# Kernel optimization log

Measured on AMD Instinct MI355X. Metric: run time of the kernel, lower is better.

The kernel has to match this reference:

```python
import jax, jax.numpy as jnp
import numpy as np

B, CIN, MID, OUT = 4096, 64, 256, 256
K = CIN * 25  # flattened 5x5 patch per channel
EPS = 1e-5


def _masks():
    # [3, 25] binary masks over the 5x5 kernel for the 3 branch families
    circle = np.zeros((5, 5), np.float32); circle[1:4, 1:4] = 1.0
    corner = np.zeros((5, 5), np.float32)
    for (i, j) in [(0, 0), (0, 4), (4, 0), (4, 4), (2, 2)]:
        corner[i, j] = 1.0
    horse = np.zeros((5, 5), np.float32)
    for (i, j) in [(0, 1), (0, 3), (1, 0), (1, 4), (3, 0), (3, 4), (4, 1), (4, 3), (2, 2)]:
        horse[i, j] = 1.0
    return jnp.asarray(np.stack([circle, corner, horse]).reshape(3, 25))


def mish(x):
    return x * jnp.tanh(jax.nn.softplus(x))


def setup_inputs() -> dict:
    key = jax.random.key(0)
    ks = jax.random.split(key, 12)
    x = jax.random.normal(ks[0], (B, CIN, 7, 7), jnp.float32)
    W5 = jax.random.normal(ks[1], (27, MID, K), jnp.float32) * 0.05
    b5 = jax.random.normal(ks[2], (27, MID), jnp.float32) * 0.05
    gamma = jnp.ones((27, MID), jnp.float32)
    beta = jnp.zeros((27, MID), jnp.float32)
    run_mean = jax.random.normal(ks[3], (27, MID), jnp.float32) * 0.05
    run_var = jax.random.uniform(ks[4], (27, MID), jnp.float32, 0.5, 1.5)
    W1 = jax.random.normal(ks[5], (27, MID, MID), jnp.float32) * 0.05
    b1 = jax.random.normal(ks[6], (27, MID), jnp.float32) * 0.05
    W2 = jax.random.normal(ks[7], (27, OUT, MID), jnp.float32) * 0.05
    b2 = jax.random.normal(ks[8], (27, OUT), jnp.float32) * 0.05
    return {"x": x, "W5": W5, "b5": b5, "gamma": gamma, "beta": beta,
            "run_mean": run_mean, "run_var": run_var,
            "W1": W1, "b1": b1, "W2": W2, "b2": b2}


def reference(x, W5, b5, gamma, beta, run_mean, run_var, W1, b1, W2, b2):
    masks = _masks()  # [3,25]
    # 9 patches of 5x5: [9, B, CIN*25]
    patches = jnp.stack([x[:, :, k:k + 5, v:v + 5]
                         for k in range(3) for v in range(3)])
    patches = patches.reshape(9, B, K)
    # mask kernels per branch family and group weights as [3,9,MID,K]
    mask_k = jnp.repeat(masks, 9, axis=0)          # [27,25]
    mask_k = jnp.tile(mask_k, (1, CIN))[:, None, :]  # [27,1,CIN*25]
    W5m = (W5 * mask_k).reshape(3, 9, MID, K)
    # masked 5x5 conv on 5x5 patch -> 1x1 == dot product: [3,9,B,MID]
    z = jnp.einsum('pbk,gpmk->gpbm', patches, W5m) + b5.reshape(3, 9, 1, MID)
    # BatchNorm (inference, running stats) + Mish
    inv = jax.lax.rsqrt(run_var.reshape(3, 9, 1, MID) + EPS)
    h = mish((z - run_mean.reshape(3, 9, 1, MID)) * inv
             * gamma.reshape(3, 9, 1, MID) + beta.reshape(3, 9, 1, MID))
    # 1x1 conv + Mish, then final 1x1 conv
    h = mish(jnp.einsum('gpbm,gpnm->gpbn', h, W1.reshape(3, 9, MID, MID))
             + b1.reshape(3, 9, 1, MID))
    o = jnp.einsum('gpbm,gpom->gpbo', h, W2.reshape(3, 9, OUT, MID)) \
        + b2.reshape(3, 9, 1, OUT)                 # [3,9,B,OUT]
    copy_features = o[0].sum(0)                    # sum of 9 circle branches
    jump_features = o[1].sum(0) + o[2].sum(0)      # sum of 18 corner+horse
    # output is 1x1 spatially, so flatten(2).sum(2) is identity on [B,OUT]
    return copy_features * jump_features
```

## Files before the change

kernel.cpp:

```cpp
#include <hip/hip_runtime.h>

typedef __bf16 bf16x8 __attribute__((ext_vector_type(8)));
typedef float f32x4 __attribute__((ext_vector_type(4)));

__constant__ int SL_I[3][9] = {{1,1,1,2,2,2,3,3,3},{0,0,2,4,4,0,0,0,0},{0,0,1,1,2,3,3,4,4}};
__constant__ int SL_J[3][9] = {{1,2,3,1,2,3,1,2,3},{0,4,2,0,4,0,0,0,0},{1,3,0,4,2,0,4,1,3}};
__constant__ int SL_S[3][9] = {{6,7,8,11,12,13,16,17,18},{0,4,12,20,24,0,0,0,0},{1,3,5,9,12,15,19,21,23}};

#define GLDS16(gsrc, ldst)                                                        \
  __builtin_amdgcn_global_load_lds(                                               \
      (const __attribute__((address_space(1))) unsigned int*)(gsrc),              \
      (__attribute__((address_space(3))) unsigned int*)(ldst), 16, 0, 0)

#define SBAR()  asm volatile("s_barrier" ::: "memory")
#define VMW(n)  asm volatile("s_waitcnt vmcnt(" #n ")" ::: "memory")
#define SCB()   __builtin_amdgcn_sched_barrier(0)

static __device__ __forceinline__ unsigned short f2b(float f) {
  return __builtin_bit_cast(unsigned short, (__bf16)f);
}
static __device__ __forceinline__ float b2f(unsigned short u) {
  unsigned int b = ((unsigned int)u) << 16;
  return __builtin_bit_cast(float, b);
}
static __device__ __forceinline__ float mish_f(float x) {
  float u = __expf(x);
  float w = u * (u + 2.0f);
  float r = x * w * __builtin_amdgcn_rcpf(w + 2.0f);
  return (x > 20.0f) ? x : r;
}
static __device__ __forceinline__ int swz8(int c, int r) {
  return ((((c >> 3) ^ (r & 7)) << 3) | (c & 7));
}
static __device__ __forceinline__ int swoff(int c, int r) {
  return (c & ~63) | ((c & 63) ^ ((r & 7) << 3));
}

__global__ __launch_bounds__(256) void prep_x_k(const float* __restrict__ X,
                                                unsigned short* __restrict__ Xb) {
  __shared__ float tile[3136];
  const int b = blockIdx.x;
  const float* xp = X + (size_t)b * 3136;
  for (int i = threadIdx.x; i < 3136; i += 256) tile[i] = xp[i];
  __syncthreads();
  for (int i = threadIdx.x; i < 3136; i += 256) {
    int s = i >> 6, c = i & 63;
    Xb[(size_t)s * 262144 + (size_t)b * 64 + swz8(c, b)] = f2b(tile[c * 49 + s]);
  }
}

__global__ __launch_bounds__(256) void prep_w5_k(const float* __restrict__ W5,
                                                 unsigned short* __restrict__ W5c) {
  int tid = blockIdx.x * 256 + threadIdx.x;
  if (tid >= 497664) return;
  int n  = tid & 127;
  int r1 = tid >> 7;
  int q  = r1 & 7;
  int r2 = r1 >> 3;
  int nt = r2 & 1;
  int r3 = r2 >> 1;
  int u  = r3 % 9;
  int gp = r3 / 9;
  int g = gp / 9;
  int nm = (g == 1) ? 5 : 9;
  if (u >= nm) return;
  int s = SL_S[g][u];
  const float* src = W5 + (size_t)(gp * 256 + nt * 128 + n) * 1600 + s;
  unsigned short* dst = W5c + (size_t)tid * 8;
  float a0 = src[(q * 8 + 0) * 25], a1 = src[(q * 8 + 1) * 25];
  float a2 = src[(q * 8 + 2) * 25], a3 = src[(q * 8 + 3) * 25];
  float a4 = src[(q * 8 + 4) * 25], a5 = src[(q * 8 + 5) * 25];
  float a6 = src[(q * 8 + 6) * 25], a7 = src[(q * 8 + 7) * 25];
  ushort4 v0 = {f2b(a0), f2b(a1), f2b(a2), f2b(a3)};
  ushort4 v1 = {f2b(a4), f2b(a5), f2b(a6), f2b(a7)};
  *(ushort4*)(dst) = v0;
  *(ushort4*)(dst + 4) = v1;
}

__global__ __launch_bounds__(256) void prep_w12_k(const float* __restrict__ W1, const float* __restrict__ W2,
                                                  unsigned short* __restrict__ W1c, unsigned short* __restrict__ W2c) {
  int tid = blockIdx.x * 256 + threadIdx.x;
  if (tid >= 221184) return;
  int n  = tid & 255;
  int q  = (tid >> 8) & 3;
  int kt = (tid >> 10) & 7;
  int gp = tid >> 13;
  size_t src = (size_t)(gp * 256 + n) * 256 + kt * 32 + q * 8;
  float4 a0 = *(const float4*)(W1 + src);
  float4 a1 = *(const float4*)(W1 + src + 4);
  float4 b0 = *(const float4*)(W2 + src);
  float4 b1 = *(const float4*)(W2 + src + 4);
  ushort4 ua0 = {f2b(a0.x), f2b(a0.y), f2b(a0.z), f2b(a0.w)};
  ushort4 ua1 = {f2b(a1.x), f2b(a1.y), f2b(a1.z), f2b(a1.w)};
  ushort4 ub0 = {f2b(b0.x), f2b(b0.y), f2b(b0.z), f2b(b0.w)};
  ushort4 ub1 = {f2b(b1.x), f2b(b1.y), f2b(b1.z), f2b(b1.w)};
  *(ushort4*)(W1c + (size_t)tid * 8) = ua0;
  *(ushort4*)(W1c + (size_t)tid * 8 + 4) = ua1;
  *(ushort4*)(W2c + (size_t)tid * 8) = ub0;
  *(ushort4*)(W2c + (size_t)tid * 8 + 4) = ub1;
}

__global__ __launch_bounds__(256) void prep_bn_k(const float* __restrict__ b5, const float* __restrict__ gamma,
                                                 const float* __restrict__ beta, const float* __restrict__ rmean,
                                                 const float* __restrict__ rvar,
                                                 float* __restrict__ bn_a, float* __restrict__ bn_c) {
  int i = blockIdx.x * 256 + threadIdx.x;
  if (i < 27 * 256) {
    float a = gamma[i] * rsqrtf(rvar[i] + 1e-5f);
    bn_a[i] = a;
    bn_c[i] = (b5[i] - rmean[i]) * a + beta[i];
  }
}

__global__ __launch_bounds__(512) void gemm1_k(const unsigned short* __restrict__ Xb,
                                               const unsigned short* __restrict__ W5c,
                                               const float* __restrict__ bn_a, const float* __restrict__ bn_c,
                                               unsigned short* __restrict__ H) {
  __shared__ unsigned short smem[32768];
  const int t = threadIdx.x;
  const int lane = t & 63;
  const int w = t >> 6;
  const int wm = w >> 2, wn = w & 3;
  const int l15 = lane & 15, l4 = lane >> 4;
  const int sw = l15 & 7;
  const int m0 = blockIdx.x * 128, n0 = blockIdx.y * 128;
  const int nt = blockIdx.y;
  const int gp = blockIdx.z;
  const int g = gp / 9, p = gp - g * 9;
  const int pk = p / 3, pv = p - pk * 3;
  const int nm = (g == 1) ? 5 : 9;

  const f32x4 zero = {0.f, 0.f, 0.f, 0.f};
  f32x4 acc[4][2];
#pragma unroll
  for (int i = 0; i < 4; ++i)
#pragma unroll
    for (int j = 0; j < 2; ++j) acc[i][j] = zero;

  auto STAGE = [&](int pbuf, int u) {
    const int s = (pk + SL_I[g][u]) * 7 + (pv + SL_J[g][u]);
    const unsigned short* srcA = Xb + (size_t)s * 262144 + (size_t)m0 * 64;
    const unsigned short* srcB = W5c + ((size_t)((gp * 9 + u) * 2 + nt)) * 8192;
    unsigned short* dA = smem + pbuf * 16384;
    unsigned short* dB = dA + 8192;
#pragma unroll
    for (int it = 0; it < 2; ++it) {
      int idx = it * 512 + t;
      GLDS16(srcA + idx * 8, dA + idx * 8);
    }
#pragma unroll
    for (int it = 0; it < 2; ++it) {
      int idx = it * 512 + t;
      GLDS16(srcB + idx * 8, dB + idx * 8);
    }
  };

  STAGE(0, 0);
  __syncthreads();
  int cur = 0;
  for (int u = 0; u < nm; ++u) {
    if (u + 1 < nm) STAGE(cur ^ 1, u + 1);
    const unsigned short* lA = smem + cur * 16384;
    const unsigned short* lB = lA + 8192;
#pragma unroll
    for (int kk = 0; kk < 2; ++kk) {
      bf16x8 af[4], bfr[2];
#pragma unroll
      for (int f4 = 0; f4 < 4; ++f4)
        af[f4] = *reinterpret_cast<const bf16x8*>(lA + (wm * 64 + f4 * 16 + l15) * 64 + (((kk * 4 + l4) ^ sw) << 3));
#pragma unroll
      for (int f2 = 0; f2 < 2; ++f2)
        bfr[f2] = *reinterpret_cast<const bf16x8*>(lB + (kk * 4 + l4) * 1024 + (wn * 32 + f2 * 16 + l15) * 8);
#pragma unroll
      for (int i = 0; i < 4; ++i)
#pragma unroll
        for (int j = 0; j < 2; ++j)
          acc[i][j] = __builtin_amdgcn_mfma_f32_16x16x32_bf16(af[i], bfr[j], acc[i][j], 0, 0, 0);
    }
    __syncthreads();
    cur ^= 1;
  }
#pragma unroll
  for (int j = 0; j < 2; ++j) {
    const int col = wn * 32 + j * 16 + l15;
    const float a  = bn_a[gp * 256 + n0 + col];
    const float cc = bn_c[gp * 256 + n0 + col];
#pragma unroll
    for (int i = 0; i < 4; ++i) {
      const int r0 = wm * 64 + i * 16 + l4 * 4;
#pragma unroll
      for (int e = 0; e < 4; ++e) {
        const int r = r0 + e;
        float z = acc[i][j][e] * a + cc;
        smem[r * 128 + (col ^ ((r & 7) << 3))] = f2b(mish_f(z));
      }
    }
  }
  __syncthreads();
  {
    unsigned short* Hg = H + (size_t)gp * 1048576;
#pragma unroll
    for (int it = 0; it < 4; ++it) {
      int idx = it * 512 + t;
      int row = idx >> 4, seg = idx & 15;
      int c8 = (seg * 8) ^ ((row & 7) << 3);
      uint4 v = *(const uint4*)(smem + row * 128 + c8);
      int colout = n0 + (seg >> 3) * 64 + (((seg & 7) ^ (row & 7)) << 3);
      *(uint4*)(Hg + (size_t)(m0 + row) * 256 + colout) = v;
    }
  }
}

__global__ __launch_bounds__(512) void gemm23f_k(const unsigned short* __restrict__ Hb,
                                                 const unsigned short* __restrict__ W1c,
                                                 const unsigned short* __restrict__ W2c,
                                                 const float* __restrict__ b1, const float* __restrict__ b2,
                                                 unsigned short* __restrict__ Obuf) {
  extern __shared__ unsigned short smem[];
  unsigned short* stB = smem;
  unsigned short* stA = smem + 24576;
  unsigned short* h1  = smem + 24576;
  const int t = threadIdx.x;
  const int lane = t & 63;
  const int w = t >> 6;
  const int wm = w >> 2, wn = w & 3;
  const int l15 = lane & 15, l4 = lane >> 4;
  const int sw = l15 & 7;
  const int m0 = blockIdx.x * 64;
  const int gp = blockIdx.y;

  const f32x4 zero = {0.f, 0.f, 0.f, 0.f};
  f32x4 acc[2][4];
#pragma unroll
  for (int i = 0; i < 2; ++i)
#pragma unroll
    for (int j = 0; j < 4; ++j) acc[i][j] = zero;

  auto STAGE_A = [&](int pbuf, int kt64) {
    unsigned short* dA = stA + pbuf * 4096;
    GLDS16(Hb + (size_t)(gp * 4096 + m0 + (t >> 3)) * 256 + kt64 * 64 + (t & 7) * 8, dA + t * 8);
  };
  auto STAGE_B = [&](const unsigned short* Wc, int kt32, int pbuf) {
    unsigned short* dB = stB + pbuf * 8192;
    const unsigned short* src = Wc + ((size_t)(gp * 8 + kt32)) * 8192;
#pragma unroll
    for (int it = 0; it < 2; ++it) {
      int idx = it * 512 + t;
      GLDS16(src + idx * 8, dB + idx * 8);
    }
  };

  STAGE_A(0, 0);
  STAGE_B(W1c, 0, 0);
#pragma unroll
  for (int kt = 0; kt < 8; ++kt) {
    if (kt < 7) STAGE_B(W1c, kt + 1, (kt + 1) % 3);
    if ((kt & 1) == 0 && kt < 6) STAGE_A((kt / 2 + 1) % 3, kt / 2 + 1);
    if (kt < 6) { VMW(3); } else if (kt == 6) { VMW(2); } else { VMW(0); }
    SBAR(); SCB();
    const unsigned short* lA = stA + ((kt >> 1) % 3) * 4096;
    const unsigned short* lB = stB + (kt % 3) * 8192;
    bf16x8 af[2], bfr[4];
#pragma unroll
    for (int f2 = 0; f2 < 2; ++f2)
      af[f2] = *reinterpret_cast<const bf16x8*>(lA + (wm * 32 + f2 * 16 + l15) * 64 + ((((kt & 1) * 4 + l4) ^ sw) << 3));
#pragma unroll
    for (int f4 = 0; f4 < 4; ++f4)
      bfr[f4] = *reinterpret_cast<const bf16x8*>(lB + l4 * 2048 + (wn * 64 + f4 * 16 + l15) * 8);
#pragma unroll
    for (int i = 0; i < 2; ++i)
#pragma unroll
      for (int j = 0; j < 4; ++j)
        acc[i][j] = __builtin_amdgcn_mfma_f32_16x16x32_bf16(af[i], bfr[j], acc[i][j], 0, 0, 0);
  }
  __syncthreads();
  STAGE_B(W2c, 0, 0);
#pragma unroll
  for (int j = 0; j < 4; ++j) {
    const int c = wn * 64 + j * 16 + l15;
    const float bi = b1[gp * 256 + c];
#pragma unroll
    for (int i = 0; i < 2; ++i) {
      const int r0 = wm * 32 + i * 16 + l4 * 4;
#pragma unroll
      for (int e = 0; e < 4; ++e) {
        const int r = r0 + e;
        h1[r * 256 + swoff(c, r)] = f2b(mish_f(acc[i][j][e] + bi));
      }
    }
  }
  __syncthreads();

#pragma unroll
  for (int i = 0; i < 2; ++i)
#pragma unroll
    for (int j = 0; j < 4; ++j) acc[i][j] = zero;
#pragma unroll
  for (int kt = 0; kt < 8; ++kt) {
    if (kt < 7) STAGE_B(W2c, kt + 1, (kt + 1) % 3);
    if (kt < 7) { VMW(2); } else { VMW(0); }
    SBAR(); SCB();
    const unsigned short* lB = stB + (kt % 3) * 8192;
    bf16x8 af[2], bfr[4];
#pragma unroll
    for (int f2 = 0; f2 < 2; ++f2) {
      const int row = wm * 32 + f2 * 16 + l15;
      af[f2] = *reinterpret_cast<const bf16x8*>(
          h1 + row * 256 + (kt >> 1) * 64 + ((((kt & 1) * 4 + l4) ^ sw) << 3));
    }
#pragma unroll
    for (int f4 = 0; f4 < 4; ++f4)
      bfr[f4] = *reinterpret_cast<const bf16x8*>(lB + l4 * 2048 + (wn * 64 + f4 * 16 + l15) * 8);
#pragma unroll
    for (int i = 0; i < 2; ++i)
#pragma unroll
      for (int j = 0; j < 4; ++j)
        acc[i][j] = __builtin_amdgcn_mfma_f32_16x16x32_bf16(af[i], bfr[j], acc[i][j], 0, 0, 0);
  }
  __syncthreads();
  unsigned short* tr = stB;
#pragma unroll
  for (int j = 0; j < 4; ++j) {
    const int c = wn * 64 + j * 16 + l15;
    const float bi = b2[gp * 256 + c];
#pragma unroll
    for (int i = 0; i < 2; ++i) {
      const int r0 = wm * 32 + i * 16 + l4 * 4;
#pragma unroll
      for (int e = 0; e < 4; ++e) {
        const int r = r0 + e;
        tr[r * 256 + swoff(c, r)] = f2b(acc[i][j][e] + bi);
      }
    }
  }
  __syncthreads();
  {
    unsigned short* Og = Obuf + (size_t)gp * 1048576;
#pragma unroll
    for (int it = 0; it < 4; ++it) {
      int idx = it * 512 + t;
      int row = idx >> 5, seg = idx & 31;
      int c8 = swoff(seg * 8, row);
      uint4 v = *(const uint4*)(tr + row * 256 + c8);
      *(uint4*)(Og + (size_t)(m0 + row) * 256 + seg * 8) = v;
    }
  }
}

__global__ __launch_bounds__(256) void final_k(const unsigned short* __restrict__ O, float* __restrict__ out) {
  const size_t base = ((size_t)blockIdx.x * 256 + threadIdx.x) * 8;
  float cs[8], js[8];
#pragma unroll
  for (int e = 0; e < 8; ++e) { cs[e] = 0.f; js[e] = 0.f; }
#pragma unroll
  for (int gp = 0; gp < 27; ++gp) {
    uint4 v = *(const uint4*)(O + (size_t)gp * 1048576 + base);
    const unsigned short* pv = (const unsigned short*)&v;
    if (gp < 9) {
#pragma unroll
      for (int e = 0; e < 8; ++e) cs[e] += b2f(pv[e]);
    } else {
#pragma unroll
      for (int e = 0; e < 8; ++e) js[e] += b2f(pv[e]);
    }
  }
  float4 o0 = {cs[0] * js[0], cs[1] * js[1], cs[2] * js[2], cs[3] * js[3]};
  float4 o1 = {cs[4] * js[4], cs[5] * js[5], cs[6] * js[6], cs[7] * js[7]};
  *(float4*)(out + base) = o0;
  *(float4*)(out + base + 4) = o1;
}

extern "C" void kernel_launch(void* const* d_in, const int* in_sizes, int n_in,
                              void* d_out, int out_size, void* d_ws, size_t ws_size,
                              hipStream_t stream) {
  const float* X     = (const float*)d_in[0];
  const float* W5    = (const float*)d_in[1];
  const float* b5    = (const float*)d_in[2];
  const float* gamma = (const float*)d_in[3];
  const float* beta  = (const float*)d_in[4];
  const float* rmean = (const float*)d_in[5];
  const float* rvar  = (const float*)d_in[6];
  const float* W1    = (const float*)d_in[7];
  const float* b1    = (const float*)d_in[8];
  const float* W2    = (const float*)d_in[9];
  const float* b2    = (const float*)d_in[10];
  float* out = (float*)d_out;
  char* ws = (char*)d_ws;

  unsigned short* W5c  = (unsigned short*)(ws);
  unsigned short* W1c  = (unsigned short*)(ws + 7962624);
  unsigned short* W2c  = (unsigned short*)(ws + 11501568);
  float*          bn_a = (float*)(ws + 15040512);
  float*          bn_c = (float*)(ws + 15068160);
  unsigned short* Xb   = (unsigned short*)(ws + 15095808);
  unsigned short* Hbuf = (unsigned short*)(ws + 40785920);
  unsigned short* Obuf = (unsigned short*)(ws + 97409024);

  (void)hipFuncSetAttribute(reinterpret_cast<const void*>(gemm23f_k),
                            hipFuncAttributeMaxDynamicSharedMemorySize, 81920);

  prep_x_k<<<4096, 256, 0, stream>>>(X, Xb);
  prep_w5_k<<<1944, 256, 0, stream>>>(W5, W5c);
  prep_w12_k<<<864, 256, 0, stream>>>(W1, W2, W1c, W2c);
  prep_bn_k<<<27, 256, 0, stream>>>(b5, gamma, beta, rmean, rvar, bn_a, bn_c);

  gemm1_k<<<dim3(32, 2, 27), 512, 0, stream>>>(Xb, W5c, bn_a, bn_c, Hbuf);
  gemm23f_k<<<dim3(64, 27), 512, 81920, stream>>>(Hbuf, W1c, W2c, b1, b2, Obuf);
  final_k<<<512, 256, 0, stream>>>(Obuf, out);
}
```

Baseline: 159.4 us.

## Split gemm1 K-steps into half-tiles with triple-buffered LDS and vmcnt waits

The prep kernel now writes X in a k-major blocked layout (8-element k-chunks by row) instead of a swizzled row-major layout, so each half-K slice of an A tile is contiguous. In gemm1 each 64-wide K step is split into two 32-wide stages, each loaded with a single global_load_lds per thread into a three-slot LDS ring. It waits on vmcnt with one s_barrier per stage instead of two __syncthreads per double-buffered step. This aims to overlap loads with MFMAs more finely and cut LDS use. It adds more barriers per unit of work and drops the XOR swizzle on A reads, which may bring back bank conflicts.

```diff
diff --git a/kernel.cpp b/kernel.cpp
--- a/kernel.cpp
+++ b/kernel.cpp
@@ -28,9 +28,6 @@
   float w = u * (u + 2.0f);
   float r = x * w * __builtin_amdgcn_rcpf(w + 2.0f);
   return (x > 20.0f) ? x : r;
-}
-static __device__ __forceinline__ int swz8(int c, int r) {
-  return ((((c >> 3) ^ (r & 7)) << 3) | (c & 7));
 }
 static __device__ __forceinline__ int swoff(int c, int r) {
   return (c & ~63) | ((c & 63) ^ ((r & 7) << 3));
@@ -43,9 +40,18 @@
   const float* xp = X + (size_t)b * 3136;
   for (int i = threadIdx.x; i < 3136; i += 256) tile[i] = xp[i];
   __syncthreads();
-  for (int i = threadIdx.x; i < 3136; i += 256) {
-    int s = i >> 6, c = i & 63;
-    Xb[(size_t)s * 262144 + (size_t)b * 64 + swz8(c, b)] = f2b(tile[c * 49 + s]);
+  const int mt = b >> 7, mr = b & 127;
+  for (int i = threadIdx.x; i < 392; i += 256) {
+    int s = i >> 3, oc = i & 7;
+    unsigned short* dst = Xb + ((size_t)((s * 32 + mt) * 8 + oc)) * 1024 + mr * 8;
+    ushort4 v0, v1;
+    int c = oc * 8;
+    v0 = {f2b(tile[(c + 0) * 49 + s]), f2b(tile[(c + 1) * 49 + s]),
+          f2b(tile[(c + 2) * 49 + s]), f2b(tile[(c + 3) * 49 + s])};
+    v1 = {f2b(tile[(c + 4) * 49 + s]), f2b(tile[(c + 5) * 49 + s]),
+          f2b(tile[(c + 6) * 49 + s]), f2b(tile[(c + 7) * 49 + s])};
+    *(ushort4*)(dst) = v0;
+    *(ushort4*)(dst + 4) = v1;
   }
 }
 
@@ -116,19 +122,21 @@
                                                const unsigned short* __restrict__ W5c,
                                                const float* __restrict__ bn_a, const float* __restrict__ bn_c,
                                                unsigned short* __restrict__ H) {
-  __shared__ unsigned short smem[32768];
+  __shared__ unsigned short smem[24576];
   const int t = threadIdx.x;
   const int lane = t & 63;
   const int w = t >> 6;
   const int wm = w >> 2, wn = w & 3;
   const int l15 = lane & 15, l4 = lane >> 4;
-  const int sw = l15 & 7;
-  const int m0 = blockIdx.x * 128, n0 = blockIdx.y * 128;
+  const int mt = blockIdx.x;
+  const int m0 = mt * 128;
   const int nt = blockIdx.y;
+  const int n0 = nt * 128;
   const int gp = blockIdx.z;
   const int g = gp / 9, p = gp - g * 9;
   const int pk = p / 3, pv = p - pk * 3;
   const int nm = (g == 1) ? 5 : 9;
+  const int S = 2 * nm;
 
   const f32x4 zero = {0.f, 0.f, 0.f, 0.f};
   f32x4 acc[4][2];
@@ -137,49 +145,37 @@
 #pragma unroll
     for (int j = 0; j < 2; ++j) acc[i][j] = zero;
 
-  auto STAGE = [&](int pbuf, int u) {
+  auto STAGE = [&](int pbuf, int st) {
+    const int u = st >> 1, kh = st & 1;
     const int s = (pk + SL_I[g][u]) * 7 + (pv + SL_J[g][u]);
-    const unsigned short* srcA = Xb + (size_t)s * 262144 + (size_t)m0 * 64;
-    const unsigned short* srcB = W5c + ((size_t)((gp * 9 + u) * 2 + nt)) * 8192;
-    unsigned short* dA = smem + pbuf * 16384;
-    unsigned short* dB = dA + 8192;
-#pragma unroll
-    for (int it = 0; it < 2; ++it) {
-      int idx = it * 512 + t;
-      GLDS16(srcA + idx * 8, dA + idx * 8);
-    }
-#pragma unroll
-    for (int it = 0; it < 2; ++it) {
-      int idx = it * 512 + t;
-      GLDS16(srcB + idx * 8, dB + idx * 8);
-    }
+    const unsigned short* srcA = Xb + ((size_t)((s * 32 + mt) * 2 + kh)) * 4096;
+    const unsigned short* srcB = W5c + ((size_t)((gp * 9 + u) * 2 + nt)) * 8192 + kh * 4096;
+    unsigned short* dA = smem + pbuf * 8192;
+    unsigned short* dB = dA + 4096;
+    GLDS16(srcA + t * 8, dA + t * 8);
+    GLDS16(srcB + t * 8, dB + t * 8);
   };
 
   STAGE(0, 0);
-  __syncthreads();
-  int cur = 0;
-  for (int u = 0; u < nm; ++u) {
-    if (u + 1 < nm) STAGE(cur ^ 1, u + 1);
-    const unsigned short* lA = smem + cur * 16384;
-    const unsigned short* lB = lA + 8192;
-#pragma unroll
-    for (int kk = 0; kk < 2; ++kk) {
-      bf16x8 af[4], bfr[2];
-#pragma unroll
-      for (int f4 = 0; f4 < 4; ++f4)
-        af[f4] = *reinterpret_cast<const bf16x8*>(lA + (wm * 64 + f4 * 16 + l15) * 64 + (((kk * 4 + l4) ^ sw) << 3));
-#pragma unroll
-      for (int f2 = 0; f2 < 2; ++f2)
-        bfr[f2] = *reinterpret_cast<const bf16x8*>(lB + (kk * 4 + l4) * 1024 + (wn * 32 + f2 * 16 + l15) * 8);
-#pragma unroll
-      for (int i = 0; i < 4; ++i)
-#pragma unroll
-        for (int j = 0; j < 2; ++j)
-          acc[i][j] = __builtin_amdgcn_mfma_f32_16x16x32_bf16(af[i], bfr[j], acc[i][j], 0, 0, 0);
-    }
-    __syncthreads();
-    cur ^= 1;
-  }
+  for (int st = 0; st < S; ++st) {
+    if (st + 1 < S) { STAGE((st + 1) % 3, st + 1); VMW(2); } else { VMW(0); }
+    SBAR(); SCB();
+    const unsigned short* lA = smem + (st % 3) * 8192;
+    const unsigned short* lB = lA + 4096;
+    bf16x8 af[4], bfr[2];
+#pragma unroll
+    for (int f4 = 0; f4 < 4; ++f4)
+      af[f4] = *reinterpret_cast<const bf16x8*>(lA + l4 * 1024 + (wm * 64 + f4 * 16 + l15) * 8);
+#pragma unroll
+    for (int f2 = 0; f2 < 2; ++f2)
+      bfr[f2] = *reinterpret_cast<const bf16x8*>(lB + l4 * 1024 + (wn * 32 + f2 * 16 + l15) * 8);
+#pragma unroll
+    for (int i = 0; i < 4; ++i)
+#pragma unroll
+      for (int j = 0; j < 2; ++j)
+        acc[i][j] = __builtin_amdgcn_mfma_f32_16x16x32_bf16(af[i], bfr[j], acc[i][j], 0, 0, 0);
+  }
+  __syncthreads();
 #pragma unroll
   for (int j = 0; j < 2; ++j) {
     const int col = wn * 32 + j * 16 + l15;
```

After: 177.8 us. 1.12x slower.
